# Kernel optimization log

Measured on AMD Instinct MI355X. Metric: run time of the kernel, lower is better.

Reference implementation:

```python
import jax, jax.numpy as jnp
import numpy as np

N_NODES = 20000
N_EDGES = 640000
NODE_NF = 64
HIDDEN = 256
N_LAYERS = 4


def _linear_init(key, fan_in, fan_out, layers=None):
    shape = (fan_in, fan_out) if layers is None else (layers, fan_in, fan_out)
    scale = 1.0 / np.sqrt(fan_in)
    return jax.random.normal(key, shape, dtype=jnp.float32) * scale


def setup_inputs() -> dict:
    key = jax.random.key(0)
    ks = jax.random.split(key, 16)
    L, H = N_LAYERS, HIDDEN
    return {
        "h": jax.random.normal(ks[0], (N_NODES, NODE_NF), dtype=jnp.float32),
        "edge_index": jax.random.randint(ks[1], (2, N_EDGES), 0, N_NODES, dtype=jnp.int64),
        "coord_diff": jax.random.normal(ks[2], (N_EDGES, 3), dtype=jnp.float32),
        # embedding in / out
        "w_in": _linear_init(ks[3], NODE_NF, H),
        "b_in": jnp.zeros((H,), jnp.float32),
        "w_out": _linear_init(ks[4], H, NODE_NF),
        "b_out": jnp.zeros((NODE_NF,), jnp.float32),
        # per-layer edge MLP: Linear(2H+1 -> H), silu, Linear(H -> H), silu
        "edge_w1": _linear_init(ks[5], 2 * H + 1, H, L),
        "edge_b1": jnp.zeros((L, H), jnp.float32),
        "edge_w2": _linear_init(ks[6], H, H, L),
        "edge_b2": jnp.zeros((L, H), jnp.float32),
        # per-layer node MLP: Linear(2H -> H), silu, Linear(H -> H)
        "node_w1": _linear_init(ks[7], 2 * H, H, L),
        "node_b1": jnp.zeros((L, H), jnp.float32),
        "node_w2": _linear_init(ks[8], H, H, L),
        "node_b2": jnp.zeros((L, H), jnp.float32),
    }


def reference(h, edge_index, coord_diff, w_in, b_in, w_out, b_out,
              edge_w1, edge_b1, edge_w2, edge_b2,
              node_w1, node_b1, node_w2, node_b2):
    row, col = edge_index[0], edge_index[1]
    # radial is layer-independent: [E, 1]
    radial = jnp.sum(coord_diff ** 2, axis=1, keepdims=True)

    h = h @ w_in + b_in  # [N, H]
    n_nodes = h.shape[0]

    for l in range(N_LAYERS):
        # edge model: gather endpoints, concat with radial, 2-layer MLP
        m = jnp.concatenate([h[row], h[col], radial], axis=1)  # [E, 2H+1]
        m = jax.nn.silu(m @ edge_w1[l] + edge_b1[l])
        m = jax.nn.silu(m @ edge_w2[l] + edge_b2[l])  # [E, H]
        # node model: segment-sum aggregate over row, concat, 2-layer MLP
        agg = jax.ops.segment_sum(m, row, num_segments=n_nodes)  # [N, H]
        x = jnp.concatenate([h, agg], axis=1)  # [N, 2H]
        x = jax.nn.silu(x @ node_w1[l] + node_b1[l])
        h = x @ node_w2[l] + node_b2[l]  # recurrent=False: no residual

    return h @ w_out + b_out  # [N, node_nf]
```

## Files before the change

kernel.cpp:

```cpp
#include <hip/hip_runtime.h>
#include <hip/hip_bf16.h>
#include <cstdint>
#include <cstddef>

#define NN 20000
#define NE 640000
#define NF 64
#define HD 256
#define NL 4
#define HTS 640

typedef __attribute__((ext_vector_type(8))) short short8;
typedef __attribute__((ext_vector_type(4))) float f32x4;
typedef __attribute__((ext_vector_type(2))) float f32x2;

__device__ __forceinline__ float bf2f(unsigned short u){
  union { unsigned int i; float f; } x; x.i = ((unsigned int)u) << 16; return x.f;
}
__device__ __forceinline__ unsigned short f2bf(float f){
  union { float f; unsigned int i; } x; x.f = f;
  unsigned int r = x.i + 0x7FFFu + ((x.i >> 16) & 1u);
  return (unsigned short)(r >> 16);
}
__device__ __forceinline__ unsigned int pk2bf(float a, float b){
  union { __hip_bfloat162 h; unsigned int u; } cv;
  cv.h = __float22bfloat162_rn(float2{a, b});
  return cv.u;
}
__device__ __forceinline__ float silu_f(float v){
  float e = __builtin_amdgcn_exp2f(v * -1.442695041f);
  return v * __builtin_amdgcn_rcpf(1.0f + e);
}
__device__ __forceinline__ f32x2 silu2(f32x2 v){
  f32x2 t = v * (f32x2){-1.442695041f, -1.442695041f};
  f32x2 e = (f32x2){__builtin_amdgcn_exp2f(t.x), __builtin_amdgcn_exp2f(t.y)};
  f32x2 d = e + (f32x2){1.0f, 1.0f};
  f32x2 r = (f32x2){__builtin_amdgcn_rcpf(d.x), __builtin_amdgcn_rcpf(d.y)};
  return v * r;
}
__device__ __forceinline__ void async16(const void* g, void* l){
  __builtin_amdgcn_global_load_lds(
      (const __attribute__((address_space(1))) unsigned int*)g,
      (__attribute__((address_space(3))) unsigned int*)l, 16, 0, 0);
}

__global__ __launch_bounds__(256) void prep_small(
    const float* __restrict__ w_in, const float* __restrict__ w_out,
    const float* __restrict__ ew1, const float* __restrict__ ew2,
    const float* __restrict__ nw1, const float* __restrict__ nw2,
    const float* __restrict__ eb1,
    unsigned short* __restrict__ w_in_t, unsigned short* __restrict__ w_out_t,
    unsigned short* __restrict__ ew1cat, float* __restrict__ w1r,
    float* __restrict__ b1e,
    unsigned short* __restrict__ ew2t, unsigned short* __restrict__ nw1t,
    unsigned short* __restrict__ nw2t)
{
  const int s = blockIdx.y;
  const int tid = blockIdx.x * 256 + threadIdx.x;
  if (s == 18) {
    if (tid < NL * 512) {
      int l = tid >> 9, c = tid & 511;
      b1e[tid] = (c < 256) ? eb1[l * HD + c] : 0.0f;
    }
    return;
  }
  if (s >= 2 && s < 6) {
    int l = s - 2;
    if (tid >= 513 * HD) return;
    int k = tid / HD, n = tid - k * HD;
    float v = ew1[(size_t)l * 513 * HD + tid];
    if (k == 512) { w1r[l * HD + n] = v; return; }
    unsigned short* dst = ew1cat + (size_t)l * 512 * 256;
    if (k < 256) dst[(size_t)n * 256 + k] = f2bf(v);
    else         dst[(size_t)(256 + n) * 256 + (k - 256)] = f2bf(v);
    return;
  }
  const float* src; unsigned short* dst; int K, N;
  if (s == 0)      { src = w_in;  dst = w_in_t;  K = NF;   N = HD; }
  else if (s == 1) { src = w_out; dst = w_out_t; K = HD;   N = NF; }
  else if (s < 10) { int l = s-6;  src = ew2 + (size_t)l*HD*HD;   dst = ew2t + (size_t)l*HD*HD;  K = HD;   N = HD; }
  else if (s < 14) { int l = s-10; src = nw1 + (size_t)l*2*HD*HD; dst = nw1t + (size_t)l*HD*512; K = 2*HD; N = HD; }
  else             { int l = s-14; src = nw2 + (size_t)l*HD*HD;   dst = nw2t + (size_t)l*HD*HD;  K = HD;   N = HD; }
  if (tid >= K * N) return;
  int k = tid / N, n = tid - k * N;
  dst[(size_t)n * K + k] = f2bf(src[tid]);
}

__global__ __launch_bounds__(256) void prep_big(
    const float* __restrict__ h_in, const float* __restrict__ cd,
    unsigned short* __restrict__ hb_in, float* __restrict__ radial)
{
  const int s = blockIdx.y;
  const int tid = blockIdx.x * 256 + threadIdx.x;
  if (s == 0) {
    if (tid < NN * NF) hb_in[tid] = f2bf(h_in[tid]);
  } else {
    if (tid < NE) {
      float x = cd[tid*3+0], y = cd[tid*3+1], z = cd[tid*3+2];
      radial[tid] = x*x + y*y + z*z;
    }
  }
}

__global__ __launch_bounds__(256) void hist_k(const int* __restrict__ erow, int* __restrict__ hist){
  int e = blockIdx.x * 256 + threadIdx.x;
  if (e < NE){
    unsigned r = (unsigned)erow[e]; if (r >= NN) r = 0;
    atomicAdd(&hist[r], 1);
  }
}

__global__ __launch_bounds__(256) void scan_k(const int* __restrict__ hist,
                                              int* __restrict__ starts, int* __restrict__ cursor){
  __shared__ int part[256];
  const int t = threadIdx.x;
  const int CH = 79;
  int lo = t * CH, hi = lo + CH; if (hi > NN) hi = NN; if (lo > NN) lo = NN;
  int s = 0;
  for (int i = lo; i < hi; ++i) s += hist[i];
  part[t] = s; __syncthreads();
  for (int off = 1; off < 256; off <<= 1){
    int v = (t >= off) ? part[t - off] : 0;
    __syncthreads();
    part[t] += v;
    __syncthreads();
  }
  int base = (t == 0) ? 0 : part[t - 1];
  for (int i = lo; i < hi; ++i){ starts[i] = base; cursor[i] = base; base += hist[i]; }
  if (t == 255) starts[NN] = part[255];
}

__global__ __launch_bounds__(256) void scatter_k(const int* __restrict__ erow,
                                                 const int* __restrict__ ecol,
                                                 const float* __restrict__ radial,
                                                 int* __restrict__ cursor,
                                                 int* __restrict__ rowcol,
                                                 float* __restrict__ radial_s){
  int e = blockIdx.x * 256 + threadIdx.x;
  if (e < NE){
    unsigned r = (unsigned)erow[e]; if (r >= NN) r = 0;
    unsigned c = (unsigned)ecol[e]; if (c >= NN) c = 0;
    int pos = atomicAdd(&cursor[r], 1);
    rowcol[2*pos]   = (int)r;
    rowcol[2*pos+1] = (int)c;
    radial_s[pos] = radial[e];
  }
}

__global__ __launch_bounds__(256) void gemm_k(
    const unsigned short* __restrict__ Am, const unsigned short* __restrict__ Wt,
    const float* __restrict__ bias,
    unsigned short* __restrict__ outB, float* __restrict__ outF,
    int M, int N, int K, int lda, int ldc, int fuseSilu)
{
  __shared__ __align__(16) unsigned short As[128*32];
  __shared__ __align__(16) unsigned short Bs[128*32];
  const int t = threadIdx.x;
  const int lane = t & 63, wave = t >> 6;
  const int ln15 = lane & 15, q = lane >> 4;
  const int bm = blockIdx.x, bn = blockIdx.y;
  const int wm = wave >> 1, wn = wave & 1;

  f32x4 acc[4][4];
  #pragma unroll
  for (int i = 0; i < 4; ++i)
    #pragma unroll
    for (int j = 0; j < 4; ++j) acc[i][j] = (f32x4){0.f,0.f,0.f,0.f};

  const int sr = t >> 2;
  const int sc = (t & 3) * 8;
  int am0 = bm*128 + sr;      if (am0 > M-1) am0 = M-1;
  int am1 = bm*128 + 64 + sr; if (am1 > M-1) am1 = M-1;
  int an0 = bn*128 + sr;      if (an0 > N-1) an0 = N-1;
  int an1 = bn*128 + 64 + sr; if (an1 > N-1) an1 = N-1;
  const unsigned short* a0 = Am + (size_t)am0 * lda + sc;
  const unsigned short* a1 = Am + (size_t)am1 * lda + sc;
  const unsigned short* b0 = Wt + (size_t)an0 * K + sc;
  const unsigned short* b1 = Wt + (size_t)an1 * K + sc;

  const int nkt = K >> 5;
  for (int kt = 0; kt < nkt; ++kt) {
    const int k0 = kt * 32;
    async16(a0 + k0, &As[t*8]);
    async16(a1 + k0, &As[2048 + t*8]);
    async16(b0 + k0, &Bs[t*8]);
    async16(b1 + k0, &Bs[2048 + t*8]);
    __syncthreads();
    short8 fa[4], fb[4];
    #pragma unroll
    for (int i = 0; i < 4; ++i)
      fa[i] = *(const short8*)&As[(wm*64 + i*16 + ln15)*32 + q*8];
    #pragma unroll
    for (int j = 0; j < 4; ++j)
      fb[j] = *(const short8*)&Bs[(wn*64 + j*16 + ln15)*32 + q*8];
    #pragma unroll
    for (int i = 0; i < 4; ++i)
      #pragma unroll
      for (int j = 0; j < 4; ++j)
        acc[i][j] = __builtin_amdgcn_mfma_f32_16x16x32_bf16(fa[i], fb[j], acc[i][j], 0, 0, 0);
    __syncthreads();
  }

  #pragma unroll
  for (int i = 0; i < 4; ++i) {
    #pragma unroll
    for (int j = 0; j < 4; ++j) {
      const int n = bn*128 + wn*64 + j*16 + ln15;
      if (n >= N) continue;
      const float bv = bias ? bias[n] : 0.0f;
      #pragma unroll
      for (int r = 0; r < 4; ++r) {
        const int m = bm*128 + wm*64 + i*16 + q*4 + r;
        if (m >= M) continue;
        float v = acc[i][j][r] + bv;
        if (fuseSilu) v = silu_f(v);
        if (outB) outB[(size_t)m * ldc + n] = f2bf(v);
        else      outF[(size_t)m * ldc + n] = v;
      }
    }
  }
}

__global__ __launch_bounds__(256, 3) void node_k(
    unsigned short* __restrict__ hcur,
    float* __restrict__ aggF,
    const unsigned short* __restrict__ w1t,
    const float* __restrict__ b1,
    const unsigned short* __restrict__ w2t,
    const float* __restrict__ b2,
    int M)
{
  __shared__ __align__(16) unsigned short As[64*32];
  __shared__ __align__(16) unsigned short Bs[256*32];
  __shared__ __align__(16) unsigned short x1L[8*64*32];
  const int t = threadIdx.x;
  const int lane = t & 63, wave = t >> 6;
  const int ln15 = lane & 15, q = lane >> 4;
  const int bm = blockIdx.x;
  const int sr = t >> 2;
  const int sc = (t & 3) * 8;

  const int row = bm*64 + sr;
  const int valid = (row < M);
  const int rowc = valid ? row : (M - 1);
  const unsigned short* aSrc = hcur + (size_t)rowc * HD + sc;
  float* gSrc = aggF + (size_t)rowc * HD + sc;

  float bv1[4], bv2[4];
  #pragma unroll
  for (int j = 0; j < 4; ++j) {
    bv1[j] = b1[wave*64 + j*16 + ln15];
    bv2[j] = b2[wave*64 + j*16 + ln15];
  }

  f32x4 acc[4][4];
  #pragma unroll
  for (int i = 0; i < 4; ++i)
    #pragma unroll
    for (int j = 0; j < 4; ++j) acc[i][j] = (f32x4){0.f,0.f,0.f,0.f};

  for (int kt = 0; kt < 16; ++kt) {
    if (kt < 8) {
      async16(aSrc + kt*32, &As[t*8]);
    } else {
      union { unsigned int u[4]; short8 s8; } cv;
      if (valid) {
        float* p = gSrc + (kt-8)*32;
        float4 a0 = *(const float4*)p;
        float4 a1 = *(const float4*)(p + 4);
        cv.u[0] = pk2bf(a0.x, a0.y); cv.u[1] = pk2bf(a0.z, a0.w);
        cv.u[2] = pk2bf(a1.x, a1.y); cv.u[3] = pk2bf(a1.z, a1.w);
        *(float4*)p = float4{0.f,0.f,0.f,0.f};
        *(float4*)(p + 4) = float4{0.f,0.f,0.f,0.f};
      } else {
        cv.u[0] = cv.u[1] = cv.u[2] = cv.u[3] = 0u;
      }
      *(short8*)&As[t*8] = cv.s8;
    }
    #pragma unroll
    for (int i = 0; i < 4; ++i)
      async16(w1t + (size_t)(i*64 + sr) * 512 + kt*32 + sc, &Bs[i*2048 + t*8]);
    __syncthreads();
    short8 fa[4], fb[4];
    #pragma unroll
    for (int i = 0; i < 4; ++i) fa[i] = *(const short8*)&As[(i*16 + ln15)*32 + q*8];
    #pragma unroll
    for (int j = 0; j < 4; ++j) fb[j] = *(const short8*)&Bs[(wave*64 + j*16 + ln15)*32 + q*8];
    #pragma unroll
    for (int i = 0; i < 4; ++i)
      #pragma unroll
      for (int j = 0; j < 4; ++j)
        acc[i][j] = __builtin_amdgcn_mfma_f32_16x16x32_bf16(fa[i], fb[j], acc[i][j], 0, 0, 0);
    __syncthreads();
  }

  #pragma unroll
  for (int i = 0; i < 4; ++i) {
    #pragma unroll
    for (int j = 0; j < 4; ++j) {
      const int k = wave*64 + j*16 + ln15;
      const int kt2 = k >> 5, k31 = k & 31;
      const f32x2 b2v = (f32x2){bv1[j], bv1[j]};
      f32x2 s01 = (f32x2){acc[i][j][0], acc[i][j][1]} + b2v;
      f32x2 s23 = (f32x2){acc[i][j][2], acc[i][j][3]} + b2v;
      f32x2 r01 = silu2(s01);
      f32x2 r23 = silu2(s23);
      const int r0 = i*16 + q*4;
      x1L[kt2*2048 + (r0  )*32 + k31] = f2bf(r01.x);
      x1L[kt2*2048 + (r0+1)*32 + k31] = f2bf(r01.y);
      x1L[kt2*2048 + (r0+2)*32 + k31] = f2bf(r23.x);
      x1L[kt2*2048 + (r0+3)*32 + k31] = f2bf(r23.y);
    }
  }
  #pragma unroll
  for (int i = 0; i < 4; ++i)
    #pragma unroll
    for (int j = 0; j < 4; ++j) acc[i][j] = (f32x4){0.f,0.f,0.f,0.f};

  for (int kt2 = 0; kt2 < 8; ++kt2) {
    #pragma unroll
    for (int i = 0; i < 4; ++i)
      async16(w2t + (size_t)(i*64 + sr) * 256 + kt2*32 + sc, &Bs[i*2048 + t*8]);
    __syncthreads();
    short8 fa[4], fb[4];
    #pragma unroll
    for (int i = 0; i < 4; ++i) fa[i] = *(const short8*)&x1L[kt2*2048 + (i*16 + ln15)*32 + q*8];
    #pragma unroll
    for (int j = 0; j < 4; ++j) fb[j] = *(const short8*)&Bs[(wave*64 + j*16 + ln15)*32 + q*8];
    #pragma unroll
    for (int i = 0; i < 4; ++i)
      #pragma unroll
      for (int j = 0; j < 4; ++j)
        acc[i][j] = __builtin_amdgcn_mfma_f32_16x16x32_bf16(fa[i], fb[j], acc[i][j], 0, 0, 0);
    __syncthreads();
  }

  #pragma unroll
  for (int i = 0; i < 4; ++i) {
    #pragma unroll
    for (int j = 0; j < 4; ++j) {
      const int n = wave*64 + j*16 + ln15;
      #pragma unroll
      for (int r = 0; r < 4; ++r) {
        const int m = bm*64 + i*16 + q*4 + r;
        if (m >= M) continue;
        hcur[(size_t)m * HD + n] = f2bf(acc[i][j][r] + bv2[j]);
      }
    }
  }
}

__global__ __launch_bounds__(256, 4) void edge_k(
    const unsigned short* __restrict__ hT,
    const int* __restrict__ rowcol,
    const float* __restrict__ radial_s,
    const float* __restrict__ w1r,
    const unsigned short* __restrict__ w2t,
    const float* __restrict__ b2,
    float* __restrict__ agg)
{
  __shared__ __align__(16) unsigned short MBUF[16896];
  __shared__ int   rowS[64];
  __shared__ float w1rS[256];
  unsigned short* M1  = MBUF;
  unsigned short* m2T = MBUF;

  const int t = threadIdx.x;
  const int lane = t & 63, wave = t >> 6;
  const int ln15 = lane & 15, q = lane >> 4;
  int blk = blockIdx.x;
  blk = (blk & 7) * ((int)gridDim.x >> 3) + (blk >> 3);
  const int e0 = blk * 64;
  const int sr = t >> 2;
  const int sc_swz = (((t & 3) ^ ((sr >> 1) & 3))) * 8;
  const int xq = ((q ^ ((ln15 >> 1) & 3))) * 8;

  const int2 rc = *(const int2*)(rowcol + 2*(e0 + sr));
  int rowv = 0;
  if (t < 64) rowv = rowcol[2*(e0 + t)];
  const float w1v = w1r[t];
  const float rad = radial_s[e0 + sr];

  float bv2[4];
  #pragma unroll
  for (int j = 0; j < 4; ++j) bv2[j] = b2[wave*64 + j*16 + ln15];

  const unsigned short* hr = hT + (size_t)rc.x * HTS + sc_swz;
  const unsigned short* hc = hT + (size_t)rc.y * HTS + 256 + sc_swz;

  short8 va[8], vb[8];
  #pragma unroll
  for (int ch = 0; ch < 8; ++ch) {
    va[ch] = *(const short8*)(hr + ch*32);
    vb[ch] = *(const short8*)(hc + ch*32);
  }

  if (t < 64) rowS[t] = rowv;
  w1rS[t] = w1v;

  const unsigned short* w2row[4];
  #pragma unroll
  for (int j = 0; j < 4; ++j)
    w2row[j] = w2t + (size_t)(wave*64 + j*16 + ln15) * HD + q*8;

  __syncthreads();

  const f32x2 rad2 = (f32x2){rad, rad};
  #pragma unroll
  for (int ch = 0; ch < 8; ++ch) {
    const int c0 = ch*32 + sc_swz;
    const unsigned int* ua = (const unsigned int*)&va[ch];
    const unsigned int* ub = (const unsigned int*)&vb[ch];
    union { unsigned int u[4]; short8 s; } res;
    #pragma unroll
    for (int i = 0; i < 4; ++i) {
      union { unsigned int i; float f; } alo, ahi, blo, bhi;
      alo.i = ua[i] << 16; ahi.i = ua[i] & 0xFFFF0000u;
      blo.i = ub[i] << 16; bhi.i = ub[i] & 0xFFFF0000u;
      f32x2 av = (f32x2){alo.f, ahi.f};
      f32x2 bv = (f32x2){blo.f, bhi.f};
      f32x2 wv = *(const f32x2*)&w1rS[c0 + 2*i];
      f32x2 o = av + bv;
      o = o + rad2 * wv;
      f32x2 sv = silu2(o);
      res.u[i] = pk2bf(sv.x, sv.y);
    }
    *(short8*)&M1[ch*2048 + sr*32 + (t & 3)*8] = res.s;
  }
  __syncthreads();

  f32x4 acc2[4][4];
  #pragma unroll
  for (int i = 0; i < 4; ++i)
    #pragma unroll
    for (int j = 0; j < 4; ++j) acc2[i][j] = (f32x4){0.f,0.f,0.f,0.f};

  __builtin_amdgcn_s_setprio(1);
  #pragma unroll
  for (int kt = 0; kt < 8; ++kt) {
    short8 fa[4], fb[4];
    #pragma unroll
    for (int j = 0; j < 4; ++j) fb[j] = *(const short8*)(w2row[j] + kt*32);
    #pragma unroll
    for (int i = 0; i < 4; ++i) fa[i] = *(const short8*)&M1[kt*2048 + (i*16 + ln15)*32 + xq];
    #pragma unroll
    for (int i = 0; i < 4; ++i)
      #pragma unroll
      for (int j = 0; j < 4; ++j)
        acc2[i][j] = __builtin_amdgcn_mfma_f32_16x16x32_bf16(fa[i], fb[j], acc2[i][j], 0, 0, 0);
  }
  __builtin_amdgcn_s_setprio(0);
  __syncthreads();

  #pragma unroll
  for (int i = 0; i < 4; ++i) {
    #pragma unroll
    for (int j = 0; j < 4; ++j) {
      const int n = wave*64 + j*16 + ln15;
      const f32x2 b2v = (f32x2){bv2[j], bv2[j]};
      f32x2 s01 = (f32x2){acc2[i][j][0], acc2[i][j][1]} + b2v;
      f32x2 s23 = (f32x2){acc2[i][j][2], acc2[i][j][3]} + b2v;
      f32x2 r01 = silu2(s01);
      f32x2 r23 = silu2(s23);
      const int m = i*16 + q*4;
      *(unsigned int*)&m2T[n*66 + m]     = pk2bf(r01.x, r01.y);
      *(unsigned int*)&m2T[n*66 + m + 2] = pk2bf(r23.x, r23.y);
    }
  }
  __syncthreads();

  {
    const int c = t;
    int cur = __builtin_amdgcn_readfirstlane(rowS[0]);
    float s = 0.f;
    #pragma unroll
    for (int m = 0; m < 64; m += 4) {
      unsigned int u0 = *(const unsigned int*)&m2T[c*66 + m];
      unsigned int u1 = *(const unsigned int*)&m2T[c*66 + m + 2];
      int n0 = __builtin_amdgcn_readfirstlane(rowS[m]);
      int n1 = __builtin_amdgcn_readfirstlane(rowS[m+1]);
      int n2 = __builtin_amdgcn_readfirstlane(rowS[m+2]);
      int n3 = __builtin_amdgcn_readfirstlane(rowS[m+3]);
      float f0 = bf2f((unsigned short)u0), f1 = bf2f((unsigned short)(u0 >> 16));
      float f2v = bf2f((unsigned short)u1), f3 = bf2f((unsigned short)(u1 >> 16));
      if (n0 != cur) { atomicAdd(&agg[(size_t)cur * HD + c], s); s = 0.f; cur = n0; }
      s += f0;
      if (n1 != cur) { atomicAdd(&agg[(size_t)cur * HD + c], s); s = 0.f; cur = n1; }
      s += f1;
      if (n2 != cur) { atomicAdd(&agg[(size_t)cur * HD + c], s); s = 0.f; cur = n2; }
      s += f2v;
      if (n3 != cur) { atomicAdd(&agg[(size_t)cur * HD + c], s); s = 0.f; cur = n3; }
      s += f3;
    }
    atomicAdd(&agg[(size_t)cur * HD + c], s);
  }
}

extern "C" void kernel_launch(void* const* d_in, const int* in_sizes, int n_in,
                              void* d_out, int out_size, void* d_ws, size_t ws_size,
                              hipStream_t stream)
{
  (void)in_sizes; (void)n_in; (void)out_size; (void)ws_size;
  const float* h_in  = (const float*)d_in[0];
  const int*   ei    = (const int*)d_in[1];
  const float* cd    = (const float*)d_in[2];
  const float* w_in  = (const float*)d_in[3];
  const float* b_in  = (const float*)d_in[4];
  const float* w_out = (const float*)d_in[5];
  const float* b_out = (const float*)d_in[6];
  const float* ew1   = (const float*)d_in[7];
  const float* eb1   = (const float*)d_in[8];
  const float* ew2   = (const float*)d_in[9];
  const float* eb2   = (const float*)d_in[10];
  const float* nw1   = (const float*)d_in[11];
  const float* nb1   = (const float*)d_in[12];
  const float* nw2   = (const float*)d_in[13];
  const float* nb2   = (const float*)d_in[14];
  float* out = (float*)d_out;

  char* base = (char*)d_ws;
  size_t off = 0;
  auto WS = [&](size_t bytes) -> char* {
    char* p = base + off;
    off = (off + bytes + 255) & ~(size_t)255;
    return p;
  };
  float*          radial  = (float*)WS((size_t)NE * 4);
  unsigned short* hb_in   = (unsigned short*)WS((size_t)NN * NF * 2);
  unsigned short* hcur    = (unsigned short*)WS((size_t)NN * HD * 2);
  float*          aggF    = (float*)WS((size_t)NN * HD * 4);
  unsigned short* hT      = (unsigned short*)WS((size_t)NN * HTS * 2);
  unsigned short* w_in_t  = (unsigned short*)WS((size_t)NF * HD * 2);
  unsigned short* w_out_t = (unsigned short*)WS((size_t)NF * HD * 2);
  unsigned short* ew1cat  = (unsigned short*)WS((size_t)NL * 512 * 256 * 2);
  float*          w1r     = (float*)WS((size_t)NL * HD * 4);
  float*          b1e     = (float*)WS((size_t)NL * 512 * 4);
  unsigned short* ew2t    = (unsigned short*)WS((size_t)NL * HD * HD * 2);
  unsigned short* nw1t    = (unsigned short*)WS((size_t)NL * HD * 512 * 2);
  unsigned short* nw2t    = (unsigned short*)WS((size_t)NL * HD * HD * 2);
  int*            hist    = (int*)WS((size_t)NN * 4);
  int*            starts  = (int*)WS((size_t)(NN + 1) * 4);
  int*            cursor  = (int*)WS((size_t)NN * 4);
  int*            rowcol  = (int*)WS((size_t)NE * 2 * 4);
  float*          radial_s= (float*)WS((size_t)NE * 4);

  hipMemsetAsync(hist, 0, (size_t)NN * 4, stream);
  hipMemsetAsync(aggF, 0, (size_t)NN * HD * 4, stream);
  prep_small<<<dim3(513, 19), 256, 0, stream>>>(w_in, w_out, ew1, ew2, nw1, nw2, eb1,
      w_in_t, w_out_t, ew1cat, w1r, b1e, ew2t, nw1t, nw2t);
  prep_big<<<dim3(5000, 2), 256, 0, stream>>>(h_in, cd, hb_in, radial);
  hist_k<<<NE / 256, 256, 0, stream>>>(ei, hist);
  scan_k<<<1, 256, 0, stream>>>(hist, starts, cursor);
  scatter_k<<<NE / 256, 256, 0, stream>>>(ei, ei + NE, radial, cursor, rowcol, radial_s);

  gemm_k<<<dim3(157, 2), 256, 0, stream>>>(hb_in, w_in_t, b_in, hcur, nullptr,
      NN, HD, NF, NF, HD, 0);

  for (int l = 0; l < NL; ++l) {
    gemm_k<<<dim3(157, 4), 256, 0, stream>>>(hcur, ew1cat + (size_t)l * 512 * 256,
        b1e + (size_t)l * 512, hT, nullptr, NN, 512, HD, HD, HTS, 0);
    edge_k<<<NE / 64, 256, 0, stream>>>(hT, rowcol, radial_s,
        w1r + l * HD, ew2t + (size_t)l * HD * HD, eb2 + l * HD, aggF);
    node_k<<<(NN + 63) / 64, 256, 0, stream>>>(hcur, aggF,
        nw1t + (size_t)l * HD * 512, nb1 + l * HD,
        nw2t + (size_t)l * HD * HD, nb2 + l * HD, NN);
  }

  gemm_k<<<dim3(157, 1), 256, 0, stream>>>(hcur, w_out_t, b_out, nullptr, out,
      NN, NF, HD, HD, NF, 0);
}
```

Before: 1.232 ms.

## Fuse next-layer edge projection GEMM into node kernel with 32-row tiles

The node kernel now also computes the next layer's per-node edge projection (hT = h @ ew1cat + b1e) from the freshly computed h held in LDS. This removes the separate gemm_k launch per layer and the re-read of hcur. The node tile shrinks from 64 to 32 rows, which raises the grid size and the occupancy bound to 4. Because 20000 divides by 32, the row bounds checks are dropped. The trade-offs are that the weight B tiles are now reloaded for every 32 rows, so weight traffic rises, and the edge kernel's occupancy bound is lowered from 4 to 3.

```diff
diff --git a/kernel.cpp b/kernel.cpp
--- a/kernel.cpp
+++ b/kernel.cpp
@@ -221,30 +221,32 @@
   }
 }
 
-__global__ __launch_bounds__(256, 3) void node_k(
+__global__ __launch_bounds__(256, 4) void node_k(
     unsigned short* __restrict__ hcur,
     float* __restrict__ aggF,
     const unsigned short* __restrict__ w1t,
     const float* __restrict__ b1,
     const unsigned short* __restrict__ w2t,
     const float* __restrict__ b2,
+    const unsigned short* __restrict__ w1cat_next,
+    const float* __restrict__ b1e_next,
+    unsigned short* __restrict__ hT,
     int M)
 {
-  __shared__ __align__(16) unsigned short As[64*32];
+  __shared__ __align__(16) unsigned short As[32*32];
   __shared__ __align__(16) unsigned short Bs[256*32];
-  __shared__ __align__(16) unsigned short x1L[8*64*32];
+  __shared__ __align__(16) unsigned short xL[8*32*32];
   const int t = threadIdx.x;
   const int lane = t & 63, wave = t >> 6;
   const int ln15 = lane & 15, q = lane >> 4;
   const int bm = blockIdx.x;
-  const int sr = t >> 2;
   const int sc = (t & 3) * 8;
-
-  const int row = bm*64 + sr;
-  const int valid = (row < M);
-  const int rowc = valid ? row : (M - 1);
-  const unsigned short* aSrc = hcur + (size_t)rowc * HD + sc;
-  float* gSrc = aggF + (size_t)rowc * HD + sc;
+  const int srA = (t & 127) >> 2;
+  const int srB = t >> 2;
+
+  const int rowA = bm*32 + srA;
+  const unsigned short* aSrc = hcur + (size_t)rowA * HD + sc;
+  float* gSrc = aggF + (size_t)rowA * HD + sc;
 
   float bv1[4], bv2[4];
   #pragma unroll
@@ -253,41 +255,39 @@
     bv2[j] = b2[wave*64 + j*16 + ln15];
   }
 
-  f32x4 acc[4][4];
-  #pragma unroll
-  for (int i = 0; i < 4; ++i)
+  f32x4 acc[2][4];
+  #pragma unroll
+  for (int i = 0; i < 2; ++i)
     #pragma unroll
     for (int j = 0; j < 4; ++j) acc[i][j] = (f32x4){0.f,0.f,0.f,0.f};
 
   for (int kt = 0; kt < 16; ++kt) {
-    if (kt < 8) {
-      async16(aSrc + kt*32, &As[t*8]);
-    } else {
-      union { unsigned int u[4]; short8 s8; } cv;
-      if (valid) {
+    if (t < 128) {
+      if (kt < 8) {
+        async16(aSrc + kt*32, &As[t*8]);
+      } else {
         float* p = gSrc + (kt-8)*32;
         float4 a0 = *(const float4*)p;
         float4 a1 = *(const float4*)(p + 4);
+        union { unsigned int u[4]; short8 s8; } cv;
         cv.u[0] = pk2bf(a0.x, a0.y); cv.u[1] = pk2bf(a0.z, a0.w);
         cv.u[2] = pk2bf(a1.x, a1.y); cv.u[3] = pk2bf(a1.z, a1.w);
         *(float4*)p = float4{0.f,0.f,0.f,0.f};
         *(float4*)(p + 4) = float4{0.f,0.f,0.f,0.f};
-      } else {
-        cv.u[0] = cv.u[1] = cv.u[2] = cv.u[3] = 0u;
+        *(short8*)&As[t*8] = cv.s8;
       }
-      *(short8*)&As[t*8] = cv.s8;
     }
     #pragma unroll
     for (int i = 0; i < 4; ++i)
-      async16(w1t + (size_t)(i*64 + sr) * 512 + kt*32 + sc, &Bs[i*2048 + t*8]);
-    __syncthreads();
-    short8 fa[4], fb[4];
-    #pragma unroll
-    for (int i = 0; i < 4; ++i) fa[i] = *(const short8*)&As[(i*16 + ln15)*32 + q*8];
+      async16(w1t + (size_t)(i*64 + srB) * 512 + kt*32 + sc, &Bs[i*2048 + t*8]);
+    __syncthreads();
+    short8 fa[2], fb[4];
+    #pragma unroll
+    for (int i = 0; i < 2; ++i) fa[i] = *(const short8*)&As[(i*16 + ln15)*32 + q*8];
     #pragma unroll
     for (int j = 0; j < 4; ++j) fb[j] = *(const short8*)&Bs[(wave*64 + j*16 + ln15)*32 + q*8];
     #pragma unroll
-    for (int i = 0; i < 4; ++i)
+    for (int i = 0; i < 2; ++i)
       #pragma unroll
       for (int j = 0; j < 4; ++j)
         acc[i][j] = __builtin_amdgcn_mfma_f32_16x16x32_bf16(fa[i], fb[j], acc[i][j], 0, 0, 0);
@@ -295,40 +295,40 @@
   }
 
   #pragma unroll
-  for (int i = 0; i < 4; ++i) {
+  for (int i = 0; i < 2; ++i) {
     #pragma unroll
     for (int j = 0; j < 4; ++j) {
       const int k = wave*64 + j*16 + ln15;
       const int kt2 = k >> 5, k31 = k & 31;
-      const f32x2 b2v = (f32x2){bv1[j], bv1[j]};
-      f32x2 s01 = (f32x2){acc[i][j][0], acc[i][j][1]} + b2v;
-      f32x2 s23 = (f32x2){acc[i][j][2], acc[i][j][3]} + b2v;
+      const f32x2 bb = (f32x2){bv1[j], bv1[j]};
+      f32x2 s01 = (f32x2){acc[i][j][0], acc[i][j][1]} + bb;
+      f32x2 s23 = (f32x2){acc[i][j][2], acc[i][j][3]} + bb;
       f32x2 r01 = silu2(s01);
       f32x2 r23 = silu2(s23);
       const int r0 = i*16 + q*4;
-      x1L[kt2*2048 + (r0  )*32 + k31] = f2bf(r01.x);
-      x1L[kt2*2048 + (r0+1)*32 + k31] = f2bf(r01.y);
-      x1L[kt2*2048 + (r0+2)*32 + k31] = f2bf(r23.x);
-      x1L[kt2*2048 + (r0+3)*32 + k31] = f2bf(r23.y);
-    }
-  }
-  #pragma unroll
-  for (int i = 0; i < 4; ++i)
+      xL[kt2*1024 + (r0  )*32 + k31] = f2bf(r01.x);
+      xL[kt2*1024 + (r0+1)*32 + k31] = f2bf(r01.y);
+      xL[kt2*1024 + (r0+2)*32 + k31] = f2bf(r23.x);
+      xL[kt2*1024 + (r0+3)*32 + k31] = f2bf(r23.y);
+    }
+  }
+  #pragma unroll
+  for (int i = 0; i < 2; ++i)
     #pragma unroll
     for (int j = 0; j < 4; ++j) acc[i][j] = (f32x4){0.f,0.f,0.f,0.f};
 
   for (int kt2 = 0; kt2 < 8; ++kt2) {
     #pragma unroll
     for (int i = 0; i < 4; ++i)
-      async16(w2t + (size_t)(i*64 + sr) * 256 + kt2*32 + sc, &Bs[i*2048 + t*8]);
-    __syncthreads();
-    short8 fa[4], fb[4];
-    #pragma unroll
-    for (int i = 0; i < 4; ++i) fa[i] = *(const short8*)&x1L[kt2*2048 + (i*16 + ln15)*32 + q*8];
+      async16(w2t + (size_t)(i*64 + srB) * 256 + kt2*32 + sc, &Bs[i*2048 + t*8]);
+    __syncthreads();
+    short8 fa[2], fb[4];
+    #pragma unroll
+    for (int i = 0; i < 2; ++i) fa[i] = *(const short8*)&xL[kt2*1024 + (i*16 + ln15)*32 + q*8];
     #pragma unroll
     for (int j = 0; j < 4; ++j) fb[j] = *(const short8*)&Bs[(wave*64 + j*16 + ln15)*32 + q*8];
     #pragma unroll
-    for (int i = 0; i < 4; ++i)
+    for (int i = 0; i < 2; ++i)
       #pragma unroll
       for (int j = 0; j < 4; ++j)
         acc[i][j] = __builtin_amdgcn_mfma_f32_16x16x32_bf16(fa[i], fb[j], acc[i][j], 0, 0, 0);
@@ -336,21 +336,74 @@
   }
 
   #pragma unroll
-  for (int i = 0; i < 4; ++i) {
+  for (int i = 0; i < 2; ++i) {
     #pragma unroll
     for (int j = 0; j < 4; ++j) {
       const int n = wave*64 + j*16 + ln15;
-      #pragma unroll
-      for (int r = 0; r < 4; ++r) {
-        const int m = bm*64 + i*16 + q*4 + r;
-        if (m >= M) continue;
-        hcur[(size_t)m * HD + n] = f2bf(acc[i][j][r] + bv2[j]);
+      const int kt2 = n >> 5, k31 = n & 31;
+      float v0 = acc[i][j][0] + bv2[j];
+      float v1 = acc[i][j][1] + bv2[j];
+      float v2 = acc[i][j][2] + bv2[j];
+      float v3 = acc[i][j][3] + bv2[j];
+      unsigned short h0 = f2bf(v0), h1 = f2bf(v1), h2 = f2bf(v2), h3 = f2bf(v3);
+      const int r0 = i*16 + q*4;
+      const int m0 = bm*32 + r0;
+      hcur[(size_t)(m0  ) * HD + n] = h0;
+      hcur[(size_t)(m0+1) * HD + n] = h1;
+      hcur[(size_t)(m0+2) * HD + n] = h2;
+      hcur[(size_t)(m0+3) * HD + n] = h3;
+      if (w1cat_next) {
+        xL[kt2*1024 + (r0  )*32 + k31] = h0;
+        xL[kt2*1024 + (r0+1)*32 + k31] = h1;
+        xL[kt2*1024 + (r0+2)*32 + k31] = h2;
+        xL[kt2*1024 + (r0+3)*32 + k31] = h3;
       }
     }
   }
-}
-
-__global__ __launch_bounds__(256, 4) void edge_k(
+
+  if (!w1cat_next) return;
+
+  #pragma unroll
+  for (int half = 0; half < 2; ++half) {
+    #pragma unroll
+    for (int i = 0; i < 2; ++i)
+      #pragma unroll
+      for (int j = 0; j < 4; ++j) acc[i][j] = (f32x4){0.f,0.f,0.f,0.f};
+    for (int kt2 = 0; kt2 < 8; ++kt2) {
+      #pragma unroll
+      for (int i = 0; i < 4; ++i)
+        async16(w1cat_next + (size_t)(half*256 + i*64 + srB) * 256 + kt2*32 + sc,
+                &Bs[i*2048 + t*8]);
+      __syncthreads();
+      short8 fa[2], fb[4];
+      #pragma unroll
+      for (int i = 0; i < 2; ++i) fa[i] = *(const short8*)&xL[kt2*1024 + (i*16 + ln15)*32 + q*8];
+      #pragma unroll
+      for (int j = 0; j < 4; ++j) fb[j] = *(const short8*)&Bs[(wave*64 + j*16 + ln15)*32 + q*8];
+      #pragma unroll
+      for (int i = 0; i < 2; ++i)
+        #pragma unroll
+        for (int j = 0; j < 4; ++j)
+          acc[i][j] = __builtin_amdgcn_mfma_f32_16x16x32_bf16(fa[i], fb[j], acc[i][j], 0, 0, 0);
+      __syncthreads();
+    }
+    #pragma unroll
+    for (int i = 0; i < 2; ++i) {
+      #pragma unroll
+      for (int j = 0; j < 4; ++j) {
+        const int n = half*256 + wave*64 + j*16 + ln15;
+        const float bv = b1e_next[n];
+        #pragma unroll
+        for (int r = 0; r < 4; ++r) {
+          const int m = bm*32 + i*16 + q*4 + r;
+          hT[(size_t)m * HTS + n] = f2bf(acc[i][j][r] + bv);
+        }
+      }
+    }
+  }
+}
+
+__global__ __launch_bounds__(256, 3) void edge_k(
     const unsigned short* __restrict__ hT,
     const int* __restrict__ rowcol,
     const float* __restrict__ radial_s,
@@ -555,15 +608,19 @@
 
   gemm_k<<<dim3(157, 2), 256, 0, stream>>>(hb_in, w_in_t, b_in, hcur, nullptr,
       NN, HD, NF, NF, HD, 0);
+  gemm_k<<<dim3(157, 4), 256, 0, stream>>>(hcur, ew1cat, b1e, hT, nullptr,
+      NN, 512, HD, HD, HTS, 0);
 
   for (int l = 0; l < NL; ++l) {
-    gemm_k<<<dim3(157, 4), 256, 0, stream>>>(hcur, ew1cat + (size_t)l * 512 * 256,
-        b1e + (size_t)l * 512, hT, nullptr, NN, 512, HD, HD, HTS, 0);
     edge_k<<<NE / 64, 256, 0, stream>>>(hT, rowcol, radial_s,
         w1r + l * HD, ew2t + (size_t)l * HD * HD, eb2 + l * HD, aggF);
-    node_k<<<(NN + 63) / 64, 256, 0, stream>>>(hcur, aggF,
+    const int last = (l == NL - 1);
+    node_k<<<(NN + 31) / 32, 256, 0, stream>>>(hcur, aggF,
         nw1t + (size_t)l * HD * 512, nb1 + l * HD,
-        nw2t + (size_t)l * HD * HD, nb2 + l * HD, NN);
+        nw2t + (size_t)l * HD * HD, nb2 + l * HD,
+        last ? nullptr : (ew1cat + (size_t)(l+1) * 512 * 256),
+        last ? nullptr : (b1e + (size_t)(l+1) * 512),
+        hT, NN);
   }
 
   gemm_k<<<dim3(157, 1), 256, 0, stream>>>(hcur, w_out_t, b_out, nullptr, out,
```

Result: no change. 1.224 ms (-0.6%).
